# Kernel tuning notes

Measured on AMD Instinct MI355X. Metric: run time of the kernel, lower is better.

## Reference

```python
import jax, jax.numpy as jnp
import numpy as np

B, T, C = 2, 2048, 1024
H = 16
DK = C // H


def setup_inputs() -> dict:
    key = jax.random.key(0)
    ks = jax.random.split(key, 5)
    x = jax.random.normal(ks[0], (B, T, C), dtype=jnp.float32)
    # causal mask, broadcastable to [B, H, T, T]; mask==0 -> -inf
    mask = jnp.tril(jnp.ones((T, T), dtype=jnp.int32))[None, None]
    s = 1.0 / np.sqrt(C)
    qkv_w = jax.random.normal(ks[1], (3 * C, C), dtype=jnp.float32) * s  # torch Linear layout [out,in]
    qkv_b = jnp.zeros((3 * C,), dtype=jnp.float32)
    out_w = jax.random.normal(ks[2], (C, C), dtype=jnp.float32) * s
    out_b = jnp.zeros((C,), dtype=jnp.float32)
    return {"x": x, "mask": mask, "qkv_w": qkv_w, "qkv_b": qkv_b,
            "out_w": out_w, "out_b": out_b}


def reference(x, mask, qkv_w, qkv_b, out_w, out_b):
    b, t, c = x.shape
    qkv = x @ qkv_w.T + qkv_b                       # [B,T,3C]
    qkv = qkv.reshape(b, t, 3, H, DK)
    q, k, v = qkv[:, :, 0], qkv[:, :, 1], qkv[:, :, 2]   # [B,T,H,DK]
    scores = jnp.einsum('bqhd,bkhd->bhqk', q, k) / np.sqrt(DK)
    scores = jnp.where(mask == 0, -jnp.inf, scores)
    attn_weights = jax.nn.softmax(scores, axis=-1)       # [B,H,T,T]
    attn_out = jnp.einsum('bhqk,bkhd->bqhd', attn_weights, v).reshape(b, t, c)
    out = attn_out @ out_w.T + out_b
    return out, attn_weights
```

## Files before the change

### kernel.cpp

```cpp
#include <hip/hip_runtime.h>
#include <hip/hip_bf16.h>

typedef short short8  __attribute__((ext_vector_type(8)));
typedef short short4v __attribute__((ext_vector_type(4)));
typedef __bf16 bf16x8 __attribute__((ext_vector_type(8)));
typedef float f32x4   __attribute__((ext_vector_type(4)));

__device__ __forceinline__ void mfma16(f32x4& d, short8 a, short8 b) {
    d = __builtin_amdgcn_mfma_f32_16x16x32_bf16(
            __builtin_bit_cast(bf16x8, a), __builtin_bit_cast(bf16x8, b), d, 0, 0, 0);
}

__device__ __forceinline__ unsigned short f2bf(float f) {
    union { float f; unsigned u; } a; a.f = f;
    unsigned u = a.u;
    return (unsigned short)((u + 0x7fffu + ((u >> 16) & 1u)) >> 16);
}
__device__ __forceinline__ float bf2f(unsigned short us) {
    union { unsigned u; float f; } a; a.u = ((unsigned)us) << 16;
    return a.f;
}

__global__ void cvt_all(const float* __restrict__ x, const float* __restrict__ w1,
                        const float* __restrict__ w2,
                        unsigned short* __restrict__ ox, unsigned short* __restrict__ o1,
                        unsigned short* __restrict__ o2) {
    int i = blockIdx.x * 256 + threadIdx.x;
    const float* src; unsigned short* dst; int j;
    if (i < 1048576)      { src = x;  dst = ox; j = i; }
    else if (i < 1835008) { src = w1; dst = o1; j = i - 1048576; }
    else                  { src = w2; dst = o2; j = i - 1835008; }
    float4 v = ((const float4*)src)[j];
    ushort4 o;
    o.x = f2bf(v.x); o.y = f2bf(v.y); o.z = f2bf(v.z); o.w = f2bf(v.w);
    ((ushort4*)dst)[j] = o;
}

template<int OUTBF, int VTF, int BM, int BN>
__global__ __launch_bounds__(256)
void gemm_bt(const unsigned short* __restrict__ A, const unsigned short* __restrict__ Bw,
             const float* __restrict__ bias, void* __restrict__ Cout,
             unsigned short* __restrict__ vt, unsigned short* __restrict__ khb,
             int M, int N, int K)
{
    constexpr int MM = BM / 32;
    constexpr int NN = BN / 32;
    __shared__ unsigned short As[BM * 64];
    __shared__ unsigned short Bs[BN * 64];

    const int tid  = threadIdx.x;
    const int lane = tid & 63;
    const int wid  = tid >> 6;

    const int swz  = (int)((blockIdx.x & 7) * (gridDim.x >> 3) + (blockIdx.x >> 3));
    const int nby  = M / BM;
    const int row0 = (swz % nby) * BM;
    const int col0 = (swz / nby) * BN;
    const int wr = (wid >> 1) * (BM >> 1);
    const int wc = (wid & 1) * (BN >> 1);
    const int rl = lane & 15;
    const int g  = lane >> 4;

    f32x4 acc[MM][NN] = {};

    for (int k0 = 0; k0 < K; k0 += 64) {
        __syncthreads();
#pragma unroll
        for (int rd = 0; rd < (BM >> 5); ++rd) {
            int s  = rd * 256 + tid;
            int r  = s >> 3, cs = s & 7;
            int cg = cs ^ (r & 7);
            __builtin_amdgcn_global_load_lds(
                (__attribute__((address_space(1))) void*)(A + (size_t)(row0 + r) * K + k0 + cg * 8),
                (__attribute__((address_space(3))) void*)(As + s * 8), 16, 0, 0);
        }
#pragma unroll
        for (int rd = 0; rd < (BN >> 5); ++rd) {
            int s  = rd * 256 + tid;
            int r  = s >> 3, cs = s & 7;
            int cg = cs ^ (r & 7);
            __builtin_amdgcn_global_load_lds(
                (__attribute__((address_space(1))) void*)(Bw + (size_t)(col0 + r) * K + k0 + cg * 8),
                (__attribute__((address_space(3))) void*)(Bs + s * 8), 16, 0, 0);
        }
        __syncthreads();

#pragma unroll
        for (int h = 0; h < 2; ++h) {
            short8 af[MM], bf[NN];
#pragma unroll
            for (int m = 0; m < MM; ++m) {
                int rr = wr + m * 16 + rl;
                int ch = ((h << 2) + g) ^ (rr & 7);
                af[m] = *(const short8*)(As + rr * 64 + ch * 8);
            }
#pragma unroll
            for (int n = 0; n < NN; ++n) {
                int rr = wc + n * 16 + rl;
                int ch = ((h << 2) + g) ^ (rr & 7);
                bf[n] = *(const short8*)(Bs + rr * 64 + ch * 8);
            }
#pragma unroll
            for (int m = 0; m < MM; ++m)
#pragma unroll
                for (int n = 0; n < NN; ++n)
                    mfma16(acc[m][n], af[m], bf[n]);
        }
    }

    const int b  = row0 >> 11;
    const int tg = (row0 & 2047) + wr + (g << 2);
#pragma unroll
    for (int n = 0; n < NN; ++n) {
        int col = col0 + wc + n * 16 + rl;
        float bv = bias[col];
        if (VTF && col >= 2048) {
            int hd = col - 2048;
            unsigned short* vr = vt + ((size_t)((b << 4) + (hd >> 6)) * 64 + (hd & 63)) * 2048;
#pragma unroll
            for (int m = 0; m < MM; ++m) {
                short4v p;
#pragma unroll
                for (int r = 0; r < 4; ++r) p[r] = (short)f2bf(acc[m][n][r] + bv);
                *(short4v*)(vr + tg + m * 16) = p;
            }
        } else if (VTF && col >= 1024) {
            int hd = col - 1024;
            unsigned short* kr = khb + ((size_t)((b << 4) + (hd >> 6)) << 17) + (hd & 63);
#pragma unroll
            for (int m = 0; m < MM; ++m)
#pragma unroll
                for (int r = 0; r < 4; ++r)
                    kr[(size_t)(tg + m * 16 + r) << 6] = f2bf(acc[m][n][r] + bv);
        } else if (VTF) {
#pragma unroll
            for (int m = 0; m < MM; ++m)
#pragma unroll
                for (int r = 0; r < 4; ++r)
                    ((unsigned short*)Cout)[(size_t)(row0 + wr + m * 16 + (g << 2) + r) * 1024 + col]
                        = f2bf(acc[m][n][r] + bv);
        } else {
#pragma unroll
            for (int m = 0; m < MM; ++m) {
#pragma unroll
                for (int r = 0; r < 4; ++r) {
                    int row = row0 + wr + m * 16 + (g << 2) + r;
                    float v = acc[m][n][r] + bv;
                    if (OUTBF) ((unsigned short*)Cout)[(size_t)row * N + col] = f2bf(v);
                    else       ((float*)Cout)[(size_t)row * N + col] = v;
                }
            }
        }
    }
}

__device__ __forceinline__ int S_addr(int row, int col) {
    return (row << 11) + ((((col >> 3) ^ (row & 7))) << 3) + (col & 7);
}

__global__ __launch_bounds__(256, 2)
void attn_kernel(const unsigned short* __restrict__ qbuf,
                 const unsigned short* __restrict__ khb,
                 const unsigned short* __restrict__ vt,
                 float* __restrict__ wout,
                 unsigned short* __restrict__ aout)
{
    __shared__ unsigned short Ss[16 * 2048];
    __shared__ float part[4][16];

    const int bid = (int)(((blockIdx.x & 7) << 9) + (blockIdx.x >> 3));
    const int qt = bid & 127;
    const int bh = bid >> 7;
    const int b = bh >> 4, h = bh & 15;
    const int q0 = qt << 4;
    const int tid = threadIdx.x;
    const int wid = tid >> 6;
    const int lane = tid & 63;
    const int rl = lane & 15;
    const int g  = lane >> 4;

    int nt = (qt + 4) & ~3;
    if (nt > 128) nt = 128;
    const int ntiles = nt;
    const int KPAD = ntiles << 4;

    const unsigned short* Qb = qbuf + (size_t)((b << 11) + q0) * 1024 + (h << 6);
    short8 qf0 = *(const short8*)(Qb + rl * 1024 + g * 8);
    short8 qf1 = *(const short8*)(Qb + rl * 1024 + 32 + g * 8);

    const unsigned short* Kh = khb + ((size_t)bh << 17);

    float psum[4] = {0.f, 0.f, 0.f, 0.f};

    {
        short8 ka0, ka1, kb0, kb1;
        {
            const unsigned short* kp = Kh + (size_t)((wid * 16 + rl) << 6);
            ka0 = *(const short8*)(kp + g * 8);
            ka1 = *(const short8*)(kp + 32 + g * 8);
        }
        if (wid + 4 < ntiles) {
            const unsigned short* kp = Kh + (size_t)((((wid + 4) * 16) + rl) << 6);
            kb0 = *(const short8*)(kp + g * 8);
            kb1 = *(const short8*)(kp + 32 + g * 8);
        } else { kb0 = ka0; kb1 = ka1; }
        for (int kt = wid; kt < ntiles; kt += 4) {
            short8 kc0 = ka0, kc1 = ka1;
            ka0 = kb0; ka1 = kb1;
            if (kt + 8 < ntiles) {
                const unsigned short* kp2 = Kh + (size_t)((((kt + 8) * 16) + rl) << 6);
                kb0 = *(const short8*)(kp2 + g * 8);
                kb1 = *(const short8*)(kp2 + 32 + g * 8);
            }
            f32x4 acc = {};
            __builtin_amdgcn_s_setprio(1);
            mfma16(acc, qf0, kc0);
            mfma16(acc, qf1, kc1);
            __builtin_amdgcn_s_setprio(0);
            int col = kt * 16 + rl;
#pragma unroll
            for (int r = 0; r < 4; ++r) {
                int qrow = g * 4 + r;
                float e = (col <= q0 + qrow) ? __expf(acc[r] * 0.125f) : 0.0f;
                Ss[S_addr(qrow, col)] = f2bf(e);
                psum[r] += e;
            }
        }
    }
#pragma unroll
    for (int m = 8; m; m >>= 1)
#pragma unroll
        for (int r = 0; r < 4; ++r) psum[r] += __shfl_xor(psum[r], m);
    if (rl == 0) {
#pragma unroll
        for (int r = 0; r < 4; ++r) part[wid][g * 4 + r] = psum[r];
    }
    __syncthreads();

    f32x4 p0 = {}, p1 = {};
    const unsigned short* vrow = vt + ((size_t)(bh << 6) + wid * 16 + rl) * 2048;
    const int np = KPAD >> 6;
    const int wrow = wid + (g << 2);
    const float invw = 1.0f / (part[0][wrow] + part[1][wrow] + part[2][wrow] + part[3][wrow]);
    float* worow = wout + ((size_t)bh * 2048 + q0 + wrow) * 2048;
    short8 bv0 = *(const short8*)(vrow + (g << 3));
    short8 bv1 = *(const short8*)(vrow + 32 + (g << 3));
    for (int ic = 0; ic < 32; ++ic) {
        int colb = (ic << 6) + (rl << 2);
        f32x4 o;
        if (ic < np) {
            short8 c0 = bv0, c1 = bv1;
            if (ic + 1 < np) {
                bv0 = *(const short8*)(vrow + ((ic + 1) << 6) + (g << 3));
                bv1 = *(const short8*)(vrow + ((ic + 1) << 6) + 32 + (g << 3));
            }
            int k0c = (ic << 3) + g;
            short8 a0 = *(const short8*)(Ss + (rl << 11) + ((k0c ^ (rl & 7)) << 3));
            short8 a1 = *(const short8*)(Ss + (rl << 11) + (((k0c + 4) ^ (rl & 7)) << 3));
            __builtin_amdgcn_s_setprio(1);
            mfma16(p0, a0, c0);
            mfma16(p1, a1, c1);
            __builtin_amdgcn_s_setprio(0);
            short4v sv = *(const short4v*)(Ss + S_addr(wrow, colb));
            o[0] = bf2f((unsigned short)sv[0]) * invw;
            o[1] = bf2f((unsigned short)sv[1]) * invw;
            o[2] = bf2f((unsigned short)sv[2]) * invw;
            o[3] = bf2f((unsigned short)sv[3]) * invw;
        } else {
            o[0] = 0.f; o[1] = 0.f; o[2] = 0.f; o[3] = 0.f;
        }
        __builtin_nontemporal_store(o, (f32x4*)(worow + colb));
    }

    f32x4 pacc = p0 + p1;
#pragma unroll
    for (int r = 0; r < 4; ++r) {
        int qrow = g * 4 + r;
        float inv = 1.0f / (part[0][qrow] + part[1][qrow] + part[2][qrow] + part[3][qrow]);
        float v = pacc[r] * inv;
        aout[(size_t)((b << 11) + q0 + qrow) * 1024 + (h << 6) + wid * 16 + rl] = f2bf(v);
    }
}

extern "C" void kernel_launch(void* const* d_in, const int* in_sizes, int n_in,
                              void* d_out, int out_size, void* d_ws, size_t ws_size,
                              hipStream_t stream)
{
    const float* x     = (const float*)d_in[0];
    const float* qkv_w = (const float*)d_in[2];
    const float* qkv_b = (const float*)d_in[3];
    const float* out_w = (const float*)d_in[4];
    const float* out_b = (const float*)d_in[5];

    char* ws = (char*)d_ws;
    unsigned short* xbf   = (unsigned short*)(ws);
    unsigned short* wqkv  = (unsigned short*)(ws + 8388608);
    unsigned short* woutw = (unsigned short*)(ws + 14680064);
    unsigned short* qbuf  = (unsigned short*)(ws + 16777216);
    unsigned short* vt    = (unsigned short*)(ws + 25165824);
    unsigned short* aout  = (unsigned short*)(ws + 33554432);
    unsigned short* khb   = (unsigned short*)(ws + 41943040);

    float* out  = (float*)d_out;
    float* wout = (float*)d_out + 4194304;

    cvt_all<<<8192, 256, 0, stream>>>(x, qkv_w, out_w, xbf, wqkv, woutw);

    gemm_bt<1, 1, 128, 128><<<768, 256, 0, stream>>>(xbf, wqkv, qkv_b, qbuf, vt, khb, 4096, 3072, 1024);
    attn_kernel<<<4096, 256, 0, stream>>>(qbuf, khb, vt, wout, aout);
    gemm_bt<0, 0, 64, 64><<<1024, 256, 0, stream>>>(aout, woutw, out_b, out, nullptr, nullptr, 4096, 1024, 1024);
}
```

Before: 211.6 us.

## Double-buffer GEMM LDS tiles to overlap global loads with MFMA

The GEMM kernel now keeps two LDS buffers for the A and B tiles. It issues the direct-to-LDS loads for the next K-tile before running the MFMAs on the current one, so global memory latency hides behind compute, and it needs only one barrier per iteration. It also raises wave priority around the MFMA block. In exchange the kernel uses twice the shared memory, which may lower occupancy.

```diff
diff --git a/kernel.cpp b/kernel.cpp
--- a/kernel.cpp
+++ b/kernel.cpp
@@ -19,6 +19,20 @@
 __device__ __forceinline__ float bf2f(unsigned short us) {
     union { unsigned u; float f; } a; a.u = ((unsigned)us) << 16;
     return a.f;
+}
+
+template<int ROWS>
+__device__ __forceinline__ void stage_tile(const unsigned short* __restrict__ src,
+                                           unsigned short* lds, int row0, int K, int k0, int tid) {
+#pragma unroll
+    for (int rd = 0; rd < (ROWS >> 5); ++rd) {
+        int s = rd * 256 + tid;
+        int r = s >> 3, cs = s & 7;
+        int cg = cs ^ (r & 7);
+        __builtin_amdgcn_global_load_lds(
+            (__attribute__((address_space(1))) void*)(src + (size_t)(row0 + r) * K + k0 + cg * 8),
+            (__attribute__((address_space(3))) void*)(lds + s * 8), 16, 0, 0);
+    }
 }
 
 __global__ void cvt_all(const float* __restrict__ x, const float* __restrict__ w1,
@@ -45,8 +59,8 @@
 {
     constexpr int MM = BM / 32;
     constexpr int NN = BN / 32;
-    __shared__ unsigned short As[BM * 64];
-    __shared__ unsigned short Bs[BN * 64];
+    __shared__ unsigned short As[2][BM * 64];
+    __shared__ unsigned short Bs[2][BN * 64];
 
     const int tid  = threadIdx.x;
     const int lane = tid & 63;
@@ -63,28 +77,18 @@
 
     f32x4 acc[MM][NN] = {};
 
-    for (int k0 = 0; k0 < K; k0 += 64) {
-        __syncthreads();
-#pragma unroll
-        for (int rd = 0; rd < (BM >> 5); ++rd) {
-            int s  = rd * 256 + tid;
-            int r  = s >> 3, cs = s & 7;
-            int cg = cs ^ (r & 7);
-            __builtin_amdgcn_global_load_lds(
-                (__attribute__((address_space(1))) void*)(A + (size_t)(row0 + r) * K + k0 + cg * 8),
-                (__attribute__((address_space(3))) void*)(As + s * 8), 16, 0, 0);
-        }
-#pragma unroll
-        for (int rd = 0; rd < (BN >> 5); ++rd) {
-            int s  = rd * 256 + tid;
-            int r  = s >> 3, cs = s & 7;
-            int cg = cs ^ (r & 7);
-            __builtin_amdgcn_global_load_lds(
-                (__attribute__((address_space(1))) void*)(Bw + (size_t)(col0 + r) * K + k0 + cg * 8),
-                (__attribute__((address_space(3))) void*)(Bs + s * 8), 16, 0, 0);
-        }
-        __syncthreads();
-
+    const int NT = K >> 6;
+    stage_tile<BM>(A,  As[0], row0, K, 0, tid);
+    stage_tile<BN>(Bw, Bs[0], col0, K, 0, tid);
+    asm volatile("s_waitcnt vmcnt(0)" ::: "memory");
+    __syncthreads();
+
+    int cur = 0;
+    for (int t = 0; t < NT; ++t) {
+        if (t + 1 < NT) {
+            stage_tile<BM>(A,  As[cur ^ 1], row0, K, (t + 1) << 6, tid);
+            stage_tile<BN>(Bw, Bs[cur ^ 1], col0, K, (t + 1) << 6, tid);
+        }
 #pragma unroll
         for (int h = 0; h < 2; ++h) {
             short8 af[MM], bf[NN];
@@ -92,20 +96,25 @@
             for (int m = 0; m < MM; ++m) {
                 int rr = wr + m * 16 + rl;
                 int ch = ((h << 2) + g) ^ (rr & 7);
-                af[m] = *(const short8*)(As + rr * 64 + ch * 8);
+                af[m] = *(const short8*)(As[cur] + rr * 64 + ch * 8);
             }
 #pragma unroll
             for (int n = 0; n < NN; ++n) {
                 int rr = wc + n * 16 + rl;
                 int ch = ((h << 2) + g) ^ (rr & 7);
-                bf[n] = *(const short8*)(Bs + rr * 64 + ch * 8);
-            }
+                bf[n] = *(const short8*)(Bs[cur] + rr * 64 + ch * 8);
+            }
+            __builtin_amdgcn_s_setprio(1);
 #pragma unroll
             for (int m = 0; m < MM; ++m)
 #pragma unroll
                 for (int n = 0; n < NN; ++n)
                     mfma16(acc[m][n], af[m], bf[n]);
-        }
+            __builtin_amdgcn_s_setprio(0);
+        }
+        asm volatile("s_waitcnt vmcnt(0)" ::: "memory");
+        __syncthreads();
+        cur ^= 1;
     }
 
     const int b  = row0 >> 11;
```

Result: slower. 224.6 us (+6.2%).

## Overlap zero-fill of masked attention weights with QK phase; deepen V prefetch

Applied to the files above, without the earlier changes.

Moves the stores that zero the fully masked tail of each attention-weight row out of the PV loop and interleaves them with the QK score loop, two per iteration, with any remainder flushed afterward. The PV loop now runs only over the valid column chunks. V loads are prefetched two chunks ahead and the first two are issued before the reduction barrier. The goal is to hide the large zero-write traffic behind compute and to add latency slack for V loads, at the cost of more live registers.

```diff
diff --git a/kernel.cpp b/kernel.cpp
--- a/kernel.cpp
+++ b/kernel.cpp
@@ -183,6 +183,12 @@
     if (nt > 128) nt = 128;
     const int ntiles = nt;
     const int KPAD = ntiles << 4;
+    const int np = KPAD >> 6;
+
+    const int wrow = wid + (g << 2);
+    float* worow = wout + ((size_t)bh * 2048 + q0 + wrow) * 2048;
+    const f32x4 zf4 = {0.f, 0.f, 0.f, 0.f};
+    int zc = np;
 
     const unsigned short* Qb = qbuf + (size_t)((b << 11) + q0) * 1024 + (h << 6);
     short8 qf0 = *(const short8*)(Qb + rl * 1024 + g * 8);
@@ -212,6 +218,14 @@
                 kb0 = *(const short8*)(kp2 + g * 8);
                 kb1 = *(const short8*)(kp2 + 32 + g * 8);
             }
+            if (zc < 32) {
+                __builtin_nontemporal_store(zf4, (f32x4*)(worow + (zc << 6) + (rl << 2)));
+                ++zc;
+            }
+            if (zc < 32) {
+                __builtin_nontemporal_store(zf4, (f32x4*)(worow + (zc << 6) + (rl << 2)));
+                ++zc;
+            }
             f32x4 acc = {};
             __builtin_amdgcn_s_setprio(1);
             mfma16(acc, qf0, kc0);
@@ -227,6 +241,18 @@
             }
         }
     }
+    for (; zc < 32; ++zc)
+        __builtin_nontemporal_store(zf4, (f32x4*)(worow + (zc << 6) + (rl << 2)));
+
+    const unsigned short* vrow = vt + ((size_t)(bh << 6) + wid * 16 + rl) * 2048;
+    short8 bva0 = *(const short8*)(vrow + (g << 3));
+    short8 bva1 = *(const short8*)(vrow + 32 + (g << 3));
+    short8 bvb0 = bva0, bvb1 = bva1;
+    if (np > 1) {
+        bvb0 = *(const short8*)(vrow + 64 + (g << 3));
+        bvb1 = *(const short8*)(vrow + 96 + (g << 3));
+    }
+
 #pragma unroll
     for (int m = 8; m; m >>= 1)
 #pragma unroll
@@ -238,37 +264,28 @@
     __syncthreads();
 
     f32x4 p0 = {}, p1 = {};
-    const unsigned short* vrow = vt + ((size_t)(bh << 6) + wid * 16 + rl) * 2048;
-    const int np = KPAD >> 6;
-    const int wrow = wid + (g << 2);
     const float invw = 1.0f / (part[0][wrow] + part[1][wrow] + part[2][wrow] + part[3][wrow]);
-    float* worow = wout + ((size_t)bh * 2048 + q0 + wrow) * 2048;
-    short8 bv0 = *(const short8*)(vrow + (g << 3));
-    short8 bv1 = *(const short8*)(vrow + 32 + (g << 3));
-    for (int ic = 0; ic < 32; ++ic) {
+    for (int ic = 0; ic < np; ++ic) {
+        short8 c0 = bva0, c1 = bva1;
+        bva0 = bvb0; bva1 = bvb1;
+        if (ic + 2 < np) {
+            bvb0 = *(const short8*)(vrow + ((ic + 2) << 6) + (g << 3));
+            bvb1 = *(const short8*)(vrow + ((ic + 2) << 6) + 32 + (g << 3));
+        }
+        int k0c = (ic << 3) + g;
+        short8 a0 = *(const short8*)(Ss + (rl << 11) + ((k0c ^ (rl & 7)) << 3));
+        short8 a1 = *(const short8*)(Ss + (rl << 11) + (((k0c + 4) ^ (rl & 7)) << 3));
+        __builtin_amdgcn_s_setprio(1);
+        mfma16(p0, a0, c0);
+        mfma16(p1, a1, c1);
+        __builtin_amdgcn_s_setprio(0);
         int colb = (ic << 6) + (rl << 2);
+        short4v sv = *(const short4v*)(Ss + S_addr(wrow, colb));
         f32x4 o;
-        if (ic < np) {
-            short8 c0 = bv0, c1 = bv1;
-            if (ic + 1 < np) {
-                bv0 = *(const short8*)(vrow + ((ic + 1) << 6) + (g << 3));
-                bv1 = *(const short8*)(vrow + ((ic + 1) << 6) + 32 + (g << 3));
-            }
-            int k0c = (ic << 3) + g;
-            short8 a0 = *(const short8*)(Ss + (rl << 11) + ((k0c ^ (rl & 7)) << 3));
-            short8 a1 = *(const short8*)(Ss + (rl << 11) + (((k0c + 4) ^ (rl & 7)) << 3));
-            __builtin_amdgcn_s_setprio(1);
-            mfma16(p0, a0, c0);
-            mfma16(p1, a1, c1);
-            __builtin_amdgcn_s_setprio(0);
-            short4v sv = *(const short4v*)(Ss + S_addr(wrow, colb));
-            o[0] = bf2f((unsigned short)sv[0]) * invw;
-            o[1] = bf2f((unsigned short)sv[1]) * invw;
-            o[2] = bf2f((unsigned short)sv[2]) * invw;
-            o[3] = bf2f((unsigned short)sv[3]) * invw;
-        } else {
-            o[0] = 0.f; o[1] = 0.f; o[2] = 0.f; o[3] = 0.f;
-        }
+        o[0] = bf2f((unsigned short)sv[0]) * invw;
+        o[1] = bf2f((unsigned short)sv[1]) * invw;
+        o[2] = bf2f((unsigned short)sv[2]) * invw;
+        o[3] = bf2f((unsigned short)sv[3]) * invw;
         __builtin_nontemporal_store(o, (f32x4*)(worow + colb));
     }
 
```

Result: no change. 215.3 us (+1.8%).
